# Kernel tuning notes

Measured on AMD Instinct MI355X. Metric: run time of the kernel, lower is better.

Reference implementation:

```python
import jax, jax.numpy as jnp
import numpy as np
import math

EMBED_DIM = 1024
NUM_HEADS = 16
HEAD_DIM = EMBED_DIM // NUM_HEADS  # 64
MAX_SEQ_LEN = 2048


def rope_tables(max_seq_len, dim):
    pos = jnp.arange(max_seq_len, dtype=jnp.float32)
    div_term = jnp.exp(jnp.arange(0, dim, 2, dtype=jnp.float32) * -(math.log(10000.0) / dim))
    ang = pos[:, None] * div_term[None, :]  # [S, dim//2]
    return jnp.sin(ang), jnp.cos(ang)


def apply_rope(x, sin, cos):
    # x: [B, H, S, D]; sin/cos: [max_seq, D//2]
    S = x.shape[2]
    sin = sin[:S][None, None]  # [1,1,S,D//2]
    cos = cos[:S][None, None]
    x1, x2 = jnp.split(x, 2, axis=-1)
    return jnp.concatenate([cos * x1 - sin * x2, sin * x1 + cos * x2], axis=-1)


def setup_inputs() -> dict:
    key = jax.random.key(0)
    ks = jax.random.split(key, 5)
    B, S, E = 4, 2048, EMBED_DIM
    std = 1.0 / math.sqrt(E)
    x = jax.random.normal(ks[0], (B, S, E), dtype=jnp.float32)
    Wq = jax.random.normal(ks[1], (E, E), dtype=jnp.float32) * std
    Wk = jax.random.normal(ks[2], (E, E), dtype=jnp.float32) * std
    Wv = jax.random.normal(ks[3], (E, E), dtype=jnp.float32) * std
    Wo = jax.random.normal(ks[4], (E, E), dtype=jnp.float32) * std
    return {"x": x, "Wq": Wq, "Wk": Wk, "Wv": Wv, "Wo": Wo}


def reference(x, Wq, Wk, Wv, Wo):
    B, S, E = x.shape
    H, D = NUM_HEADS, HEAD_DIM
    scale = 1.0 / math.sqrt(D)
    sin, cos = rope_tables(MAX_SEQ_LEN, D)

    def split_heads(t):
        return t.reshape(B, S, H, D).transpose(0, 2, 1, 3)  # [B,H,S,D]

    q = split_heads(x @ Wq)
    k = split_heads(x @ Wk)
    v = split_heads(x @ Wv)
    q = apply_rope(q, sin, cos)
    k = apply_rope(k, sin, cos)

    scores = jnp.einsum('bhqd,bhkd->bhqk', q, k) * scale
    causal = jnp.where(jnp.tril(jnp.ones((S, S), dtype=bool)), 0.0, -1e9)
    scores = scores + causal[None, None]
    attn = jax.nn.softmax(scores, axis=-1)
    out = jnp.einsum('bhqk,bhkd->bhqd', attn, v)  # [B,H,S,D]
    out = out.transpose(0, 2, 1, 3).reshape(B, S, E)
    return out @ Wo
```

## Files before the change

kernel.cpp:

```cpp
#include <hip/hip_runtime.h>

#define DEVFN __device__ __forceinline__

typedef __attribute__((ext_vector_type(8))) short bf16x8;
typedef __attribute__((ext_vector_type(4))) float f32x4;
typedef __attribute__((ext_vector_type(16))) float f32x16;

#define MFMA16(a, b, c) __builtin_amdgcn_mfma_f32_16x16x32_bf16(a, b, c, 0, 0, 0)
#define MFMA32(a, b, c) __builtin_amdgcn_mfma_f32_32x32x16_bf16(a, b, c, 0, 0, 0)

DEVFN unsigned short f2bf(float f) {
  union { float f; unsigned u; } v; v.f = f;
  unsigned r = v.u + 0x7FFFu + ((v.u >> 16) & 1u);
  return (unsigned short)(r >> 16);
}
DEVFN unsigned pack2bf(float a, float b) {
  return (unsigned)f2bf(a) | ((unsigned)f2bf(b) << 16);
}
DEVFN unsigned cvtpk(float lo, float hi) {
  unsigned r;
  asm("v_cvt_pk_bf16_f32 %0, %1, %2" : "=v"(r) : "v"(lo), "v"(hi));
  return r;
}
DEVFN void pl32swap(unsigned& a, unsigned& b) {
  asm("v_permlane32_swap_b32 %0, %1" : "+v"(a), "+v"(b));
}
DEVFN void gll16(const void* g, void* l) {
  __builtin_amdgcn_global_load_lds((__attribute__((address_space(1))) void*)g,
                                   (__attribute__((address_space(3))) void*)l,
                                   16, 0, 0);
}


__global__ __launch_bounds__(256) void conv_x_k(const float* __restrict__ x,
                                                unsigned short* __restrict__ xb) {
  int i = (blockIdx.x * 256 + threadIdx.x) * 4;
  float4 v = *(const float4*)(x + i);
  uint2 u;
  u.x = pack2bf(v.x, v.y);
  u.y = pack2bf(v.z, v.w);
  *(uint2*)(xb + i) = u;
}

__global__ __launch_bounds__(256) void transp_k(
    const float* __restrict__ Wq, const float* __restrict__ Wk,
    const float* __restrict__ Wv, const float* __restrict__ Wo,
    unsigned short* __restrict__ Tq, unsigned short* __restrict__ Tk,
    unsigned short* __restrict__ Tv, unsigned short* __restrict__ To) {
  __shared__ unsigned short t[64 * 65];
  int z = blockIdx.z;
  const float* src = (z == 0) ? Wq : (z == 1) ? Wk : (z == 2) ? Wv : Wo;
  unsigned short* dst = (z == 0) ? Tq : (z == 1) ? Tk : (z == 2) ? Tv : To;
  int k0 = blockIdx.x * 64, n0 = blockIdx.y * 64;
  int tid = threadIdx.x;
#pragma unroll
  for (int i = 0; i < 16; ++i) {
    int flat = i * 256 + tid;
    int r = flat >> 6, cc = flat & 63;
    t[cc * 65 + r] = f2bf(src[(size_t)(k0 + r) * 1024 + n0 + cc]);
  }
  __syncthreads();
#pragma unroll
  for (int i = 0; i < 16; ++i) {
    int flat = i * 256 + tid;
    int rr = flat >> 6, cc = flat & 63;
    dst[(size_t)(n0 + rr) * 1024 + k0 + cc] = t[rr * 65 + cc];
  }
}

__global__ __launch_bounds__(256) void rope_k(float2* __restrict__ rtab) {
  int idx = blockIdx.x * 256 + threadIdx.x;
  int s = idx >> 5, j = idx & 31;
  float freq = expf(-0.28782313714981824f * (float)j);
  float ang = (float)s * freq;
  rtab[idx] = make_float2(sinf(ang), cosf(ang));
}

__global__ __launch_bounds__(256) void gemm_qkv_k(
    const unsigned short* __restrict__ A, const unsigned short* __restrict__ WTq,
    const unsigned short* __restrict__ WTk, const unsigned short* __restrict__ WTv,
    unsigned short* __restrict__ Qb, unsigned short* __restrict__ Kfb,
    unsigned short* __restrict__ Vfb, const float2* __restrict__ rtab) {
  __shared__ unsigned short At[128 * 64];
  __shared__ unsigned short Bt[128 * 64];
  const int tid = threadIdx.x;
  const int w = tid >> 6, lane = tid & 63, g = lane >> 4, c = lane & 15;
  const int wr = w >> 1, wc = w & 1;
  const int which = blockIdx.y >> 3;
  const unsigned short* WT = (which == 0) ? WTq : (which == 1) ? WTk : WTv;
  const int m0 = blockIdx.x * 128, n0 = (blockIdx.y & 7) * 128;

  f32x4 zero = {0.f, 0.f, 0.f, 0.f};
  f32x4 acc[4][4];
#pragma unroll
  for (int i = 0; i < 4; ++i)
#pragma unroll
    for (int j = 0; j < 4; ++j) acc[i][j] = zero;

  for (int k0 = 0; k0 < 1024; k0 += 64) {
#pragma unroll
    for (int p = 0; p < 4; ++p) {
      int i = p * 256 + tid;
      int row = i >> 3, ls = i & 7;
      size_t off = ((size_t)(m0 + row) * 1024 + k0) * 2 + ((ls ^ (row & 7)) << 4);
      gll16((const char*)A + off, (char*)At + p * 4096 + w * 1024);
      size_t offb = ((size_t)(n0 + row) * 1024 + k0) * 2 + ((ls ^ (row & 7)) << 4);
      gll16((const char*)WT + offb, (char*)Bt + p * 4096 + w * 1024);
    }
    __syncthreads();
#pragma unroll
    for (int ks = 0; ks < 2; ++ks) {
      bf16x8 af[4], bfv[4];
#pragma unroll
      for (int am = 0; am < 4; ++am) {
        int row = wr * 64 + am * 16 + c;
        af[am] = *(const bf16x8*)(At + row * 64 + ((((ks << 2) | g) ^ (row & 7)) << 3));
      }
#pragma unroll
      for (int bn = 0; bn < 4; ++bn) {
        int row = wc * 64 + bn * 16 + c;
        bfv[bn] = *(const bf16x8*)(Bt + row * 64 + ((((ks << 2) | g) ^ (row & 7)) << 3));
      }
#pragma unroll
      for (int am = 0; am < 4; ++am)
#pragma unroll
        for (int bn = 0; bn < 4; ++bn)
          acc[am][bn] = MFMA16(af[am], bfv[bn], acc[am][bn]);
    }
    __syncthreads();
  }

  if (which == 0) {
#pragma unroll
    for (int am = 0; am < 4; ++am)
#pragma unroll
      for (int bp = 0; bp < 2; ++bp) {
        int col = n0 + wc * 64 + bp * 16 + c;
        int h = col >> 6, j = col & 63;
#pragma unroll
        for (int r = 0; r < 4; ++r) {
          int row = m0 + wr * 64 + am * 16 + (g << 2) + r;
          int b = row >> 11, s = row & 2047;
          float x1 = acc[am][bp][r], x2 = acc[am][bp + 2][r];
          float2 sc = rtab[s * 32 + j];
          float o1 = (sc.y * x1 - sc.x * x2) * 0.18033688011112042f;
          float o2 = (sc.x * x1 + sc.y * x2) * 0.18033688011112042f;
          size_t base = (((size_t)(b * 16 + h)) * 2048 + s) * 64;
          Qb[base + j] = f2bf(o1);
          Qb[base + 32 + j] = f2bf(o2);
        }
      }
  } else if (which == 1) {
#pragma unroll
    for (int am = 0; am < 4; ++am)
#pragma unroll
      for (int bp = 0; bp < 2; ++bp) {
        int col = n0 + wc * 64 + bp * 16 + c;
        int h = col >> 6, j = col & 63;
        const int kb = j >> 4, hil = (j >> 3) & 1, el = j & 7;
#pragma unroll
        for (int r = 0; r < 4; ++r) {
          int row = m0 + wr * 64 + am * 16 + (g << 2) + r;
          int b = row >> 11, s = row & 2047;
          float x1 = acc[am][bp][r], x2 = acc[am][bp + 2][r];
          float2 sc = rtab[s * 32 + j];
          float o1 = sc.y * x1 - sc.x * x2;
          float o2 = sc.x * x1 + sc.y * x2;
          size_t base = (size_t)(b * 16 + h) * 131072 + (size_t)(s >> 5) * 2048 +
                        (hil * 32 + (s & 31)) * 8 + el;
          Kfb[base + kb * 512] = f2bf(o1);
          Kfb[base + (kb + 2) * 512] = f2bf(o2);
        }
      }
  } else {
#pragma unroll
    for (int am = 0; am < 4; ++am)
#pragma unroll
      for (int bn = 0; bn < 4; ++bn) {
        int col = n0 + wc * 64 + bn * 16 + c;
        int h = col >> 6, d = col & 63;
        int row0 = m0 + wr * 64 + am * 16 + (g << 2);
        int b = row0 >> 11, s0 = row0 & 2047;
        uint2 u;
        u.x = pack2bf(acc[am][bn][0], acc[am][bn][1]);
        u.y = pack2bf(acc[am][bn][2], acc[am][bn][3]);
        size_t off = (size_t)(b * 16 + h) * 131072 + (size_t)(s0 >> 6) * 4096 +
                     ((s0 >> 4) & 3) * 1024 + (d >> 5) * 512 +
                     (((s0 >> 3) & 1) * 32 + (d & 31)) * 8 + (s0 & 7);
        *(uint2*)(Vfb + off) = u;
      }
  }
}

__global__ __launch_bounds__(256) void gemm_o_k(
    const unsigned short* __restrict__ A, const unsigned short* __restrict__ WT,
    float* __restrict__ outf) {
  __shared__ unsigned short At[128 * 64];
  __shared__ unsigned short Bt[128 * 64];
  const int tid = threadIdx.x;
  const int w = tid >> 6, lane = tid & 63, g = lane >> 4, c = lane & 15;
  const int wr = w >> 1, wc = w & 1;
  const int m0 = blockIdx.x * 128, n0 = blockIdx.y * 128;

  f32x4 zero = {0.f, 0.f, 0.f, 0.f};
  f32x4 acc[4][4];
#pragma unroll
  for (int i = 0; i < 4; ++i)
#pragma unroll
    for (int j = 0; j < 4; ++j) acc[i][j] = zero;

  for (int k0 = 0; k0 < 1024; k0 += 64) {
#pragma unroll
    for (int p = 0; p < 4; ++p) {
      int i = p * 256 + tid;
      int row = i >> 3, ls = i & 7;
      size_t off = ((size_t)(m0 + row) * 1024 + k0) * 2 + ((ls ^ (row & 7)) << 4);
      gll16((const char*)A + off, (char*)At + p * 4096 + w * 1024);
      size_t offb = ((size_t)(n0 + row) * 1024 + k0) * 2 + ((ls ^ (row & 7)) << 4);
      gll16((const char*)WT + offb, (char*)Bt + p * 4096 + w * 1024);
    }
    __syncthreads();
#pragma unroll
    for (int ks = 0; ks < 2; ++ks) {
      bf16x8 af[4], bfv[4];
#pragma unroll
      for (int am = 0; am < 4; ++am) {
        int row = wr * 64 + am * 16 + c;
        af[am] = *(const bf16x8*)(At + row * 64 + ((((ks << 2) | g) ^ (row & 7)) << 3));
      }
#pragma unroll
      for (int bn = 0; bn < 4; ++bn) {
        int row = wc * 64 + bn * 16 + c;
        bfv[bn] = *(const bf16x8*)(Bt + row * 64 + ((((ks << 2) | g) ^ (row & 7)) << 3));
      }
#pragma unroll
      for (int am = 0; am < 4; ++am)
#pragma unroll
        for (int bn = 0; bn < 4; ++bn)
          acc[am][bn] = MFMA16(af[am], bfv[bn], acc[am][bn]);
    }
    __syncthreads();
  }

#pragma unroll
  for (int am = 0; am < 4; ++am)
#pragma unroll
    for (int bn = 0; bn < 4; ++bn)
#pragma unroll
      for (int r = 0; r < 4; ++r)
        outf[(size_t)(m0 + wr * 64 + am * 16 + (g << 2) + r) * 1024 +
             (n0 + wc * 64 + bn * 16 + c)] = acc[am][bn][r];
}

__global__ __launch_bounds__(256, 2) void attn_k(
    const unsigned short* __restrict__ Q, const unsigned short* __restrict__ Kf,
    const unsigned short* __restrict__ Vf, unsigned short* __restrict__ ctx) {
  const int blk = blockIdx.x;
  const int xcd = blk & 7, j = blk >> 3;
  const int hp = j & 3;
  const int s = 31 - (j >> 2);
  const int tid = threadIdx.x;
  const int w = tid >> 6, lane = tid & 63;
  const int hi = lane >> 5, c5 = lane & 31;
  const int bh = xcd * 8 + hp * 2 + (w & 1);
  const int U = 2 * s + (w >> 1);
  const int S = s + 1;
  const int qw = U * 32;

  const unsigned short* Qbh = Q + (size_t)bh * 2048 * 64;
  const unsigned short* Kbh = Kf + (size_t)bh * 131072;
  const unsigned short* Vbh = Vf + (size_t)bh * 131072;
  const int b = bh >> 4, h = bh & 15;

  f32x16 zacc;
#pragma unroll
  for (int i = 0; i < 16; ++i) zacc[i] = 0.f;

  bf16x8 qf[4];
#pragma unroll
  for (int kb = 0; kb < 4; ++kb)
    qf[kb] = *(const bf16x8*)(Qbh + (size_t)(qw + c5) * 64 + kb * 16 + hi * 8);

  f32x16 oacc[2];
  oacc[0] = zacc; oacc[1] = zacc;
  float m_run = -1e30f, l_run = 0.f;

  bf16x8 kfA[2][4], vfA[2][4], kfB[2][4], vfB[2][4];

  auto loadK = [&](int st, bf16x8 (&dst)[2][4]) {
    const unsigned short* kb_ = Kbh + (size_t)st * 4096 + lane * 8;
#pragma unroll
    for (int t = 0; t < 2; ++t)
#pragma unroll
      for (int kb = 0; kb < 4; ++kb)
        dst[t][kb] = *(const bf16x8*)(kb_ + t * 2048 + kb * 512);
  };
  auto loadV = [&](int st, bf16x8 (&dst)[2][4]) {
    const unsigned short* vb_ = Vbh + (size_t)st * 4096 + lane * 8;
#pragma unroll
    for (int kb = 0; kb < 4; ++kb) {
      dst[0][kb] = *(const bf16x8*)(vb_ + kb * 1024);
      dst[1][kb] = *(const bf16x8*)(vb_ + kb * 1024 + 512);
    }
  };

  auto step = [&](int st, bf16x8 (&kfC)[2][4], bf16x8 (&vfC)[2][4],
                  bf16x8 (&kfN)[2][4], bf16x8 (&vfN)[2][4]) {
    f32x16 sacc[2];
    __builtin_amdgcn_s_setprio(1);
#pragma unroll
    for (int t = 0; t < 2; ++t) {
      sacc[t] = MFMA32(kfC[t][0], qf[0], zacc);
#pragma unroll
      for (int kb = 1; kb < 4; ++kb)
        sacc[t] = MFMA32(kfC[t][kb], qf[kb], sacc[t]);
    }
    __builtin_amdgcn_s_setprio(0);

    if (st + 1 < S) {
      loadK(st + 1, kfN);
      loadV(st + 1, vfN);
    }

    if (st == S - 1) {
      const int q = qw + c5;
#pragma unroll
      for (int t = 0; t < 2; ++t) {
        const int kvb = st * 64 + t * 32 + (hi << 2);
#pragma unroll
        for (int i = 0; i < 16; ++i) {
          int kv = kvb + (i & 3) + ((i >> 2) << 3);
          if (kv > q) sacc[t][i] = -1e30f;
        }
      }
    }

    float vmax = fmaxf(sacc[0][0], sacc[0][1]);
#pragma unroll
    for (int t = 0; t < 2; ++t)
#pragma unroll
      for (int i = (t == 0 ? 2 : 0); i < 16; i += 2)
        vmax = fmaxf(vmax, fmaxf(sacc[t][i], sacc[t][i + 1]));
    vmax = fmaxf(vmax, __shfl_xor(vmax, 32, 64));
    if (!__all(vmax <= m_run + 8.0f)) {
      float m_new = fmaxf(m_run, vmax);
      float alpha = exp2f(m_run - m_new);
      l_run *= alpha;
#pragma unroll
      for (int i = 0; i < 16; ++i) {
        oacc[0][i] *= alpha;
        oacc[1][i] *= alpha;
      }
      m_run = m_new;
    }
    float psum = 0.f;
#pragma unroll
    for (int t = 0; t < 2; ++t)
#pragma unroll
      for (int i = 0; i < 16; ++i) {
        float pv = exp2f(sacc[t][i] - m_run);
        sacc[t][i] = pv;
        psum += pv;
      }
    psum += __shfl_xor(psum, 32, 64);
    l_run += psum;

    unsigned pword[4][4];
#pragma unroll
    for (int t = 0; t < 2; ++t) {
      unsigned X[4][2];
#pragma unroll
      for (int u2 = 0; u2 < 4; ++u2)
#pragma unroll
        for (int wp = 0; wp < 2; ++wp)
          X[u2][wp] = cvtpk(sacc[t][u2 * 4 + 2 * wp], sacc[t][u2 * 4 + 2 * wp + 1]);
#pragma unroll
      for (int par = 0; par < 2; ++par) {
        const int kb = 2 * t + par;
#pragma unroll
        for (int wp = 0; wp < 2; ++wp) {
          unsigned a = X[2 * par][wp], b2 = X[2 * par + 1][wp];
          pl32swap(a, b2);
          pword[kb][wp] = a;
          pword[kb][wp + 2] = b2;
        }
      }
    }

    __builtin_amdgcn_s_setprio(1);
#pragma unroll
    for (int kb = 0; kb < 4; ++kb) {
      union { unsigned u[4]; bf16x8 v; } pw;
#pragma unroll
      for (int k2 = 0; k2 < 4; ++k2) pw.u[k2] = pword[kb][k2];
      oacc[0] = MFMA32(vfC[0][kb], pw.v, oacc[0]);
      oacc[1] = MFMA32(vfC[1][kb], pw.v, oacc[1]);
    }
    __builtin_amdgcn_s_setprio(0);
  };

  loadK(0, kfA);
  loadV(0, vfA);
  for (int st = 0; st < S; st += 2) {
    step(st, kfA, vfA, kfB, vfB);
    if (st + 1 < S) step(st + 1, kfB, vfB, kfA, vfA);
  }

  const float linv = 1.f / l_run;
  unsigned short* crow = ctx + ((size_t)(b * 2048 + qw + c5)) * 1024 + h * 64;
#pragma unroll
  for (int dt = 0; dt < 2; ++dt)
#pragma unroll
    for (int u = 0; u < 4; ++u) {
      int d0 = dt * 32 + 8 * u + 4 * hi;
      uint2 o;
      o.x = cvtpk(oacc[dt][4 * u] * linv, oacc[dt][4 * u + 1] * linv);
      o.y = cvtpk(oacc[dt][4 * u + 2] * linv, oacc[dt][4 * u + 3] * linv);
      *(uint2*)(crow + d0) = o;
    }
}


extern "C" void kernel_launch(void* const* d_in, const int* in_sizes, int n_in,
                              void* d_out, int out_size, void* d_ws, size_t ws_size,
                              hipStream_t stream) {
  (void)in_sizes; (void)n_in; (void)out_size; (void)ws_size;
  const float* x = (const float*)d_in[0];
  const float* Wq = (const float*)d_in[1];
  const float* Wk = (const float*)d_in[2];
  const float* Wv = (const float*)d_in[3];
  const float* Wo = (const float*)d_in[4];
  char* ws = (char*)d_ws;
  const size_t MiB = 1024 * 1024;
  unsigned short* xb  = (unsigned short*)(ws);
  unsigned short* WTq = (unsigned short*)(ws + 16 * MiB);
  unsigned short* WTk = (unsigned short*)(ws + 18 * MiB);
  unsigned short* WTv = (unsigned short*)(ws + 20 * MiB);
  unsigned short* WTo = (unsigned short*)(ws + 22 * MiB);
  unsigned short* Qb  = (unsigned short*)(ws + 24 * MiB);
  unsigned short* Kfb = (unsigned short*)(ws + 40 * MiB);
  unsigned short* Vfb = (unsigned short*)(ws + 56 * MiB);
  unsigned short* ctx = (unsigned short*)(ws + 72 * MiB);
  float2* rtab = (float2*)(ws + 88 * MiB);

  conv_x_k<<<8192, 256, 0, stream>>>(x, xb);
  transp_k<<<dim3(16, 16, 4), 256, 0, stream>>>(Wq, Wk, Wv, Wo, WTq, WTk, WTv, WTo);
  rope_k<<<256, 256, 0, stream>>>(rtab);
  gemm_qkv_k<<<dim3(64, 24), 256, 0, stream>>>(xb, WTq, WTk, WTv, Qb, Kfb, Vfb, rtab);
  attn_k<<<1024, 256, 0, stream>>>(Qb, Kfb, Vfb, ctx);
  gemm_o_k<<<dim3(64, 8), 256, 0, stream>>>(ctx, WTo, (float*)d_out);
}
```

Before: 178.1 us.

## Merge prep kernels, pair causal query tiles per wave, use permlane reductions

Three prep kernels (x cast, weight transpose, rope table) become one launch that branches on block index, saving launch overhead. The attention kernel now runs 512 blocks. Each wave handles one head and processes query tile P and then 63-P, so every wave does the same causal amount of work, replacing the earlier descending-size scheduling. Cross-half max and sum reductions use v_permlane32_swap instead of shuffles. The cost is half as many blocks and sequential passes per wave, which could reduce latency hiding.

```diff
diff --git a/kernel.cpp b/kernel.cpp
--- a/kernel.cpp
+++ b/kernel.cpp
@@ -25,55 +25,67 @@
 DEVFN void pl32swap(unsigned& a, unsigned& b) {
   asm("v_permlane32_swap_b32 %0, %1" : "+v"(a), "+v"(b));
 }
+DEVFN float halfmax(float x) {
+  unsigned a = __float_as_uint(x), b;
+  asm("v_mov_b32 %0, %1" : "=v"(b) : "v"(a));
+  pl32swap(a, b);
+  return fmaxf(__uint_as_float(a), __uint_as_float(b));
+}
+DEVFN float halfsum(float x) {
+  unsigned a = __float_as_uint(x), b;
+  asm("v_mov_b32 %0, %1" : "=v"(b) : "v"(a));
+  pl32swap(a, b);
+  return __uint_as_float(a) + __uint_as_float(b);
+}
 DEVFN void gll16(const void* g, void* l) {
   __builtin_amdgcn_global_load_lds((__attribute__((address_space(1))) void*)g,
                                    (__attribute__((address_space(3))) void*)l,
                                    16, 0, 0);
 }
 
-
-__global__ __launch_bounds__(256) void conv_x_k(const float* __restrict__ x,
-                                                unsigned short* __restrict__ xb) {
-  int i = (blockIdx.x * 256 + threadIdx.x) * 4;
-  float4 v = *(const float4*)(x + i);
-  uint2 u;
-  u.x = pack2bf(v.x, v.y);
-  u.y = pack2bf(v.z, v.w);
-  *(uint2*)(xb + i) = u;
-}
-
-__global__ __launch_bounds__(256) void transp_k(
+__global__ __launch_bounds__(256) void prep_k(
+    const float* __restrict__ x, unsigned short* __restrict__ xb,
     const float* __restrict__ Wq, const float* __restrict__ Wk,
     const float* __restrict__ Wv, const float* __restrict__ Wo,
     unsigned short* __restrict__ Tq, unsigned short* __restrict__ Tk,
-    unsigned short* __restrict__ Tv, unsigned short* __restrict__ To) {
+    unsigned short* __restrict__ Tv, unsigned short* __restrict__ To,
+    float2* __restrict__ rtab) {
   __shared__ unsigned short t[64 * 65];
-  int z = blockIdx.z;
-  const float* src = (z == 0) ? Wq : (z == 1) ? Wk : (z == 2) ? Wv : Wo;
-  unsigned short* dst = (z == 0) ? Tq : (z == 1) ? Tk : (z == 2) ? Tv : To;
-  int k0 = blockIdx.x * 64, n0 = blockIdx.y * 64;
-  int tid = threadIdx.x;
-#pragma unroll
-  for (int i = 0; i < 16; ++i) {
-    int flat = i * 256 + tid;
-    int r = flat >> 6, cc = flat & 63;
-    t[cc * 65 + r] = f2bf(src[(size_t)(k0 + r) * 1024 + n0 + cc]);
+  const int blk = blockIdx.x;
+  const int tid = threadIdx.x;
+  if (blk < 8192) {
+    int i = (blk * 256 + tid) * 4;
+    float4 v = *(const float4*)(x + i);
+    uint2 u;
+    u.x = pack2bf(v.x, v.y);
+    u.y = pack2bf(v.z, v.w);
+    *(uint2*)(xb + i) = u;
+  } else if (blk < 9216) {
+    const int lb = blk - 8192;
+    const int z = lb >> 8, by = (lb >> 4) & 15, bx = lb & 15;
+    const float* src = (z == 0) ? Wq : (z == 1) ? Wk : (z == 2) ? Wv : Wo;
+    unsigned short* dst = (z == 0) ? Tq : (z == 1) ? Tk : (z == 2) ? Tv : To;
+    int k0 = bx * 64, n0 = by * 64;
+#pragma unroll
+    for (int i = 0; i < 16; ++i) {
+      int flat = i * 256 + tid;
+      int r = flat >> 6, cc = flat & 63;
+      t[cc * 65 + r] = f2bf(src[(size_t)(k0 + r) * 1024 + n0 + cc]);
+    }
+    __syncthreads();
+#pragma unroll
+    for (int i = 0; i < 16; ++i) {
+      int flat = i * 256 + tid;
+      int rr = flat >> 6, cc = flat & 63;
+      dst[(size_t)(n0 + rr) * 1024 + k0 + cc] = t[rr * 65 + cc];
+    }
+  } else {
+    int idx = (blk - 9216) * 256 + tid;
+    int s = idx >> 5, j = idx & 31;
+    float freq = expf(-0.28782313714981824f * (float)j);
+    float ang = (float)s * freq;
+    rtab[idx] = make_float2(sinf(ang), cosf(ang));
   }
-  __syncthreads();
-#pragma unroll
-  for (int i = 0; i < 16; ++i) {
-    int flat = i * 256 + tid;
-    int rr = flat >> 6, cc = flat & 63;
-    dst[(size_t)(n0 + rr) * 1024 + k0 + cc] = t[rr * 65 + cc];
-  }
-}
-
-__global__ __launch_bounds__(256) void rope_k(float2* __restrict__ rtab) {
-  int idx = blockIdx.x * 256 + threadIdx.x;
-  int s = idx >> 5, j = idx & 31;
-  float freq = expf(-0.28782313714981824f * (float)j);
-  float ang = (float)s * freq;
-  rtab[idx] = make_float2(sinf(ang), cosf(ang));
 }
 
 __global__ __launch_bounds__(256) void gemm_qkv_k(
@@ -256,16 +268,13 @@
     const unsigned short* __restrict__ Q, const unsigned short* __restrict__ Kf,
     const unsigned short* __restrict__ Vf, unsigned short* __restrict__ ctx) {
   const int blk = blockIdx.x;
-  const int xcd = blk & 7, j = blk >> 3;
-  const int hp = j & 3;
-  const int s = 31 - (j >> 2);
+  const int xcd = blk & 7, idx = blk >> 3;
+  const int bh = (xcd << 3) + (idx & 7);
+  const int pbase = (idx >> 3) << 2;
   const int tid = threadIdx.x;
   const int w = tid >> 6, lane = tid & 63;
   const int hi = lane >> 5, c5 = lane & 31;
-  const int bh = xcd * 8 + hp * 2 + (w & 1);
-  const int U = 2 * s + (w >> 1);
-  const int S = s + 1;
-  const int qw = U * 32;
+  const int P = pbase + w;
 
   const unsigned short* Qbh = Q + (size_t)bh * 2048 * 64;
   const unsigned short* Kbh = Kf + (size_t)bh * 131072;
@@ -276,148 +285,155 @@
 #pragma unroll
   for (int i = 0; i < 16; ++i) zacc[i] = 0.f;
 
-  bf16x8 qf[4];
-#pragma unroll
-  for (int kb = 0; kb < 4; ++kb)
-    qf[kb] = *(const bf16x8*)(Qbh + (size_t)(qw + c5) * 64 + kb * 16 + hi * 8);
-
-  f32x16 oacc[2];
-  oacc[0] = zacc; oacc[1] = zacc;
-  float m_run = -1e30f, l_run = 0.f;
-
-  bf16x8 kfA[2][4], vfA[2][4], kfB[2][4], vfB[2][4];
-
-  auto loadK = [&](int st, bf16x8 (&dst)[2][4]) {
-    const unsigned short* kb_ = Kbh + (size_t)st * 4096 + lane * 8;
-#pragma unroll
-    for (int t = 0; t < 2; ++t)
-#pragma unroll
-      for (int kb = 0; kb < 4; ++kb)
-        dst[t][kb] = *(const bf16x8*)(kb_ + t * 2048 + kb * 512);
+  auto pass = [&](int U) {
+    const int qw = U * 32;
+    const int S = (U >> 1) + 1;
+
+    bf16x8 qf[4];
+#pragma unroll
+    for (int kb = 0; kb < 4; ++kb)
+      qf[kb] = *(const bf16x8*)(Qbh + (size_t)(qw + c5) * 64 + kb * 16 + hi * 8);
+
+    f32x16 oacc[2];
+    oacc[0] = zacc; oacc[1] = zacc;
+    float m_run = -1e30f, l_run = 0.f;
+
+    bf16x8 kfA[2][4], vfA[2][4], kfB[2][4], vfB[2][4];
+
+    auto loadK = [&](int st, bf16x8 (&dst)[2][4]) {
+      const unsigned short* kb_ = Kbh + (size_t)st * 4096 + lane * 8;
+#pragma unroll
+      for (int t = 0; t < 2; ++t)
+#pragma unroll
+        for (int kb = 0; kb < 4; ++kb)
+          dst[t][kb] = *(const bf16x8*)(kb_ + t * 2048 + kb * 512);
+    };
+    auto loadV = [&](int st, bf16x8 (&dst)[2][4]) {
+      const unsigned short* vb_ = Vbh + (size_t)st * 4096 + lane * 8;
+#pragma unroll
+      for (int kb = 0; kb < 4; ++kb) {
+        dst[0][kb] = *(const bf16x8*)(vb_ + kb * 1024);
+        dst[1][kb] = *(const bf16x8*)(vb_ + kb * 1024 + 512);
+      }
+    };
+
+    auto step = [&](int st, bf16x8 (&kfC)[2][4], bf16x8 (&vfC)[2][4],
+                    bf16x8 (&kfN)[2][4], bf16x8 (&vfN)[2][4]) {
+      f32x16 sacc[2];
+      __builtin_amdgcn_s_setprio(1);
+#pragma unroll
+      for (int t = 0; t < 2; ++t) {
+        sacc[t] = MFMA32(kfC[t][0], qf[0], zacc);
+#pragma unroll
+        for (int kb = 1; kb < 4; ++kb)
+          sacc[t] = MFMA32(kfC[t][kb], qf[kb], sacc[t]);
+      }
+      __builtin_amdgcn_s_setprio(0);
+
+      if (st + 1 < S) {
+        loadK(st + 1, kfN);
+        loadV(st + 1, vfN);
+      }
+
+      if (st == S - 1) {
+        const int q = qw + c5;
+#pragma unroll
+        for (int t = 0; t < 2; ++t) {
+          const int kvb = st * 64 + t * 32 + (hi << 2);
+#pragma unroll
+          for (int i = 0; i < 16; ++i) {
+            int kv = kvb + (i & 3) + ((i >> 2) << 3);
+            if (kv > q) sacc[t][i] = -1e30f;
+          }
+        }
+      }
+
+      float vmax = fmaxf(sacc[0][0], sacc[0][1]);
+#pragma unroll
+      for (int t = 0; t < 2; ++t)
+#pragma unroll
+        for (int i = (t == 0 ? 2 : 0); i < 16; i += 2)
+          vmax = fmaxf(vmax, fmaxf(sacc[t][i], sacc[t][i + 1]));
+      vmax = halfmax(vmax);
+      if (!__all(vmax <= m_run + 8.0f)) {
+        float m_new = fmaxf(m_run, vmax);
+        float alpha = exp2f(m_run - m_new);
+        l_run *= alpha;
+#pragma unroll
+        for (int i = 0; i < 16; ++i) {
+          oacc[0][i] *= alpha;
+          oacc[1][i] *= alpha;
+        }
+        m_run = m_new;
+      }
+      float psum = 0.f;
+#pragma unroll
+      for (int t = 0; t < 2; ++t)
+#pragma unroll
+        for (int i = 0; i < 16; ++i) {
+          float pv = exp2f(sacc[t][i] - m_run);
+          sacc[t][i] = pv;
+          psum += pv;
+        }
+      l_run += halfsum(psum);
+
+      unsigned pword[4][4];
+#pragma unroll
+      for (int t = 0; t < 2; ++t) {
+        unsigned X[4][2];
+#pragma unroll
+        for (int u2 = 0; u2 < 4; ++u2)
+#pragma unroll
+          for (int wp = 0; wp < 2; ++wp)
+            X[u2][wp] = cvtpk(sacc[t][u2 * 4 + 2 * wp], sacc[t][u2 * 4 + 2 * wp + 1]);
+#pragma unroll
+        for (int par = 0; par < 2; ++par) {
+          const int kb = 2 * t + par;
+#pragma unroll
+          for (int wp = 0; wp < 2; ++wp) {
+            unsigned a = X[2 * par][wp], b2 = X[2 * par + 1][wp];
+            pl32swap(a, b2);
+            pword[kb][wp] = a;
+            pword[kb][wp + 2] = b2;
+          }
+        }
+      }
+
+      __builtin_amdgcn_s_setprio(1);
+#pragma unroll
+      for (int kb = 0; kb < 4; ++kb) {
+        union { unsigned u[4]; bf16x8 v; } pw;
+#pragma unroll
+        for (int k2 = 0; k2 < 4; ++k2) pw.u[k2] = pword[kb][k2];
+        oacc[0] = MFMA32(vfC[0][kb], pw.v, oacc[0]);
+        oacc[1] = MFMA32(vfC[1][kb], pw.v, oacc[1]);
+      }
+      __builtin_amdgcn_s_setprio(0);
+    };
+
+    loadK(0, kfA);
+    loadV(0, vfA);
+    for (int st = 0; st < S; st += 2) {
+      step(st, kfA, vfA, kfB, vfB);
+      if (st + 1 < S) step(st + 1, kfB, vfB, kfA, vfA);
+    }
+
+    const float linv = 1.f / l_run;
+    unsigned short* crow = ctx + ((size_t)(b * 2048 + qw + c5)) * 1024 + h * 64;
+#pragma unroll
+    for (int dt = 0; dt < 2; ++dt)
+#pragma unroll
+      for (int u = 0; u < 4; ++u) {
+        int d0 = dt * 32 + 8 * u + 4 * hi;
+        uint2 o;
+        o.x = cvtpk(oacc[dt][4 * u] * linv, oacc[dt][4 * u + 1] * linv);
+        o.y = cvtpk(oacc[dt][4 * u + 2] * linv, oacc[dt][4 * u + 3] * linv);
+        *(uint2*)(crow + d0) = o;
+      }
   };
-  auto loadV = [&](int st, bf16x8 (&dst)[2][4]) {
-    const unsigned short* vb_ = Vbh + (size_t)st * 4096 + lane * 8;
-#pragma unroll
-    for (int kb = 0; kb < 4; ++kb) {
-      dst[0][kb] = *(const bf16x8*)(vb_ + kb * 1024);
-      dst[1][kb] = *(const bf16x8*)(vb_ + kb * 1024 + 512);
-    }
-  };
-
-  auto step = [&](int st, bf16x8 (&kfC)[2][4], bf16x8 (&vfC)[2][4],
-                  bf16x8 (&kfN)[2][4], bf16x8 (&vfN)[2][4]) {
-    f32x16 sacc[2];
-    __builtin_amdgcn_s_setprio(1);
-#pragma unroll
-    for (int t = 0; t < 2; ++t) {
-      sacc[t] = MFMA32(kfC[t][0], qf[0], zacc);
-#pragma unroll
-      for (int kb = 1; kb < 4; ++kb)
-        sacc[t] = MFMA32(kfC[t][kb], qf[kb], sacc[t]);
-    }
-    __builtin_amdgcn_s_setprio(0);
-
-    if (st + 1 < S) {
-      loadK(st + 1, kfN);
-      loadV(st + 1, vfN);
-    }
-
-    if (st == S - 1) {
-      const int q = qw + c5;
-#pragma unroll
-      for (int t = 0; t < 2; ++t) {
-        const int kvb = st * 64 + t * 32 + (hi << 2);
-#pragma unroll
-        for (int i = 0; i < 16; ++i) {
-          int kv = kvb + (i & 3) + ((i >> 2) << 3);
-          if (kv > q) sacc[t][i] = -1e30f;
-        }
-      }
-    }
-
-    float vmax = fmaxf(sacc[0][0], sacc[0][1]);
-#pragma unroll
-    for (int t = 0; t < 2; ++t)
-#pragma unroll
-      for (int i = (t == 0 ? 2 : 0); i < 16; i += 2)
-        vmax = fmaxf(vmax, fmaxf(sacc[t][i], sacc[t][i + 1]));
-    vmax = fmaxf(vmax, __shfl_xor(vmax, 32, 64));
-    if (!__all(vmax <= m_run + 8.0f)) {
-      float m_new = fmaxf(m_run, vmax);
-      float alpha = exp2f(m_run - m_new);
-      l_run *= alpha;
-#pragma unroll
-      for (int i = 0; i < 16; ++i) {
-        oacc[0][i] *= alpha;
-        oacc[1][i] *= alpha;
-      }
-      m_run = m_new;
-    }
-    float psum = 0.f;
-#pragma unroll
-    for (int t = 0; t < 2; ++t)
-#pragma unroll
-      for (int i = 0; i < 16; ++i) {
-        float pv = exp2f(sacc[t][i] - m_run);
-        sacc[t][i] = pv;
-        psum += pv;
-      }
-    psum += __shfl_xor(psum, 32, 64);
-    l_run += psum;
-
-    unsigned pword[4][4];
-#pragma unroll
-    for (int t = 0; t < 2; ++t) {
-      unsigned X[4][2];
-#pragma unroll
-      for (int u2 = 0; u2 < 4; ++u2)
-#pragma unroll
-        for (int wp = 0; wp < 2; ++wp)
-          X[u2][wp] = cvtpk(sacc[t][u2 * 4 + 2 * wp], sacc[t][u2 * 4 + 2 * wp + 1]);
-#pragma unroll
-      for (int par = 0; par < 2; ++par) {
-        const int kb = 2 * t + par;
-#pragma unroll
-        for (int wp = 0; wp < 2; ++wp) {
-          unsigned a = X[2 * par][wp], b2 = X[2 * par + 1][wp];
-          pl32swap(a, b2);
-          pword[kb][wp] = a;
-          pword[kb][wp + 2] = b2;
-        }
-      }
-    }
-
-    __builtin_amdgcn_s_setprio(1);
-#pragma unroll
-    for (int kb = 0; kb < 4; ++kb) {
-      union { unsigned u[4]; bf16x8 v; } pw;
-#pragma unroll
-      for (int k2 = 0; k2 < 4; ++k2) pw.u[k2] = pword[kb][k2];
-      oacc[0] = MFMA32(vfC[0][kb], pw.v, oacc[0]);
-      oacc[1] = MFMA32(vfC[1][kb], pw.v, oacc[1]);
-    }
-    __builtin_amdgcn_s_setprio(0);
-  };
-
-  loadK(0, kfA);
-  loadV(0, vfA);
-  for (int st = 0; st < S; st += 2) {
-    step(st, kfA, vfA, kfB, vfB);
-    if (st + 1 < S) step(st + 1, kfB, vfB, kfA, vfA);
-  }
-
-  const float linv = 1.f / l_run;
-  unsigned short* crow = ctx + ((size_t)(b * 2048 + qw + c5)) * 1024 + h * 64;
-#pragma unroll
-  for (int dt = 0; dt < 2; ++dt)
-#pragma unroll
-    for (int u = 0; u < 4; ++u) {
-      int d0 = dt * 32 + 8 * u + 4 * hi;
-      uint2 o;
-      o.x = cvtpk(oacc[dt][4 * u] * linv, oacc[dt][4 * u + 1] * linv);
-      o.y = cvtpk(oacc[dt][4 * u + 2] * linv, oacc[dt][4 * u + 3] * linv);
-      *(uint2*)(crow + d0) = o;
-    }
+
+  pass(P);
+  pass(63 - P);
 }
 
 
@@ -443,10 +459,8 @@
   unsigned short* ctx = (unsigned short*)(ws + 72 * MiB);
   float2* rtab = (float2*)(ws + 88 * MiB);
 
-  conv_x_k<<<8192, 256, 0, stream>>>(x, xb);
-  transp_k<<<dim3(16, 16, 4), 256, 0, stream>>>(Wq, Wk, Wv, Wo, WTq, WTk, WTv, WTo);
-  rope_k<<<256, 256, 0, stream>>>(rtab);
+  prep_k<<<9472, 256, 0, stream>>>(x, xb, Wq, Wk, Wv, Wo, WTq, WTk, WTv, WTo, rtab);
   gemm_qkv_k<<<dim3(64, 24), 256, 0, stream>>>(xb, WTq, WTk, WTv, Qb, Kfb, Vfb, rtab);
-  attn_k<<<1024, 256, 0, stream>>>(Qb, Kfb, Vfb, ctx);
+  attn_k<<<512, 256, 0, stream>>>(Qb, Kfb, Vfb, ctx);
   gemm_o_k<<<dim3(64, 8), 256, 0, stream>>>(ctx, WTo, (float*)d_out);
 }
```

New measurement: 175.7 us. No clear change (-1.3%).
